# Optimization experiments

Measured on AMD Instinct MI355X. Metric: run time of the kernel, lower is better.

## Reference

```python
import jax, jax.numpy as jnp
import numpy as np

B, S, D = 2, 2048, 1024
H = 16
HD = D // H  # head_dim = 64
NEG = -1e30  # finite stand-in for -inf; masked entries are zeroed after softmax so math matches


def setup_inputs() -> dict:
    key = jax.random.key(0)
    ks = jax.random.split(key, 10)
    q = jax.random.normal(ks[0], (B, S, D), dtype=jnp.float32)
    k = jax.random.normal(ks[1], (B, S, D), dtype=jnp.float32)
    v = jax.random.normal(ks[2], (B, S, D), dtype=jnp.float32)
    mask = jax.random.randint(ks[3], (B, S), 0, 2).astype(bool)
    s = 1.0 / np.sqrt(D)
    Wq = jax.random.uniform(ks[4], (D, D), jnp.float32, -s, s)
    bq = jax.random.uniform(ks[5], (D,), jnp.float32, -s, s)
    Wk = jax.random.uniform(ks[6], (D, D), jnp.float32, -s, s)
    bk = jax.random.uniform(ks[7], (D,), jnp.float32, -s, s)
    Wv = jax.random.uniform(ks[8], (D, D), jnp.float32, -s, s)
    bv = jax.random.uniform(ks[9], (D,), jnp.float32, -s, s)
    return {"q": q, "k": k, "v": v, "mask": mask,
            "Wq": Wq, "bq": bq, "Wk": Wk, "bk": bk, "Wv": Wv, "bv": bv}


def _split_heads(x):
    # [B,S,D] -> [H,B,S,HD]  (matches permute(2,0,1,3) in torch)
    return x.reshape(B, S, H, HD).transpose(2, 0, 1, 3)


def reference(q, k, v, mask, Wq, bq, Wk, bk, Wv, bv):
    mq = _split_heads(q @ Wq.T + bq)
    mk = _split_heads(k @ Wk.T + bk)
    mv = _split_heads(v @ Wv.T + bv)
    # scores: [H,B,Sq,Sk]
    scores = jnp.einsum('hbqd,hbkd->hbqk', mq, mk) / jnp.sqrt(jnp.float32(HD))
    pair_mask = (mask[:, :, None] & mask[:, None, :])[None]  # [1,B,S,S]
    scores = jnp.where(pair_mask, scores, NEG)
    attn = jax.nn.softmax(scores, axis=-1)
    attn = jnp.where(pair_mask, attn, 0.0)
    out = jnp.einsum('hbqk,hbkd->hbqd', attn, mv)
    # [H,B,S,HD] -> [B,S,D]
    return out.transpose(1, 2, 0, 3).reshape(B, S, H * HD)
```

## Files before the change

### kernel.cpp

```cpp
#include <hip/hip_runtime.h>
#include <math.h>

#define B_ 2
#define S_ 2048
#define D_ 1024
#define H_ 16
#define HD_ 64
#define LOG2E 1.44269504088896340736f

typedef __bf16 bf16_t;
typedef bf16_t bf16x8 __attribute__((ext_vector_type(8)));
typedef bf16_t bf16x4v __attribute__((ext_vector_type(4)));
typedef float f32x4 __attribute__((ext_vector_type(4)));

#define GLOBAL_LOAD_LDS16(gp, lp)                                              \
    __builtin_amdgcn_global_load_lds(                                          \
        (const __attribute__((address_space(1))) void*)(gp),                   \
        (__attribute__((address_space(3))) void*)(lp), 16, 0, 0)

__global__ __launch_bounds__(256) void cvt_kernel(
    const float* __restrict__ q, const float* __restrict__ k,
    const float* __restrict__ v, const float* __restrict__ wq,
    const float* __restrict__ wk, const float* __restrict__ wv,
    const int* __restrict__ msk,
    bf16_t* __restrict__ qb, bf16_t* __restrict__ kb, bf16_t* __restrict__ vb,
    bf16_t* __restrict__ wqb, bf16_t* __restrict__ wkb, bf16_t* __restrict__ wvb,
    float* __restrict__ kbias)
{
    const int y = blockIdx.y;
    size_t idx = ((size_t)blockIdx.x * 256 + threadIdx.x) * 4;

    if (y == 6) {
        if (idx >= (size_t)B_ * S_) return;
        int4 mi = *(const int4*)(msk + idx);
        float4 o4;
        const float VB = -8.0f * LOG2E;
        const float MB = -1.44269504e30f;
        o4.x = mi.x ? VB : MB;
        o4.y = mi.y ? VB : MB;
        o4.z = mi.z ? VB : MB;
        o4.w = mi.w ? VB : MB;
        *(float4*)(kbias + idx) = o4;
        return;
    }

    const float* src;
    bf16_t* dst;
    size_t n;
    switch (y) {
        case 0: src = q;  dst = qb;  n = (size_t)B_ * S_ * D_; break;
        case 1: src = k;  dst = kb;  n = (size_t)B_ * S_ * D_; break;
        case 2: src = v;  dst = vb;  n = (size_t)B_ * S_ * D_; break;
        case 3: src = wq; dst = wqb; n = (size_t)D_ * D_;      break;
        case 4: src = wk; dst = wkb; n = (size_t)D_ * D_;      break;
        default: src = wv; dst = wvb; n = (size_t)D_ * D_;     break;
    }
    if (idx >= n) return;
    float4 f = *(const float4*)(src + idx);
    bf16x4v o;
    o[0] = (bf16_t)f.x; o[1] = (bf16_t)f.y;
    o[2] = (bf16_t)f.z; o[3] = (bf16_t)f.w;
    *(bf16x4v*)(dst + idx) = o;
}

__global__ __launch_bounds__(256) void proj_mfma(
    const bf16_t* __restrict__ X0, const bf16_t* __restrict__ X1,
    const bf16_t* __restrict__ X2, const bf16_t* __restrict__ W0,
    const bf16_t* __restrict__ W1, const bf16_t* __restrict__ W2,
    const float* __restrict__ b0, const float* __restrict__ b1,
    const float* __restrict__ b2, bf16_t* __restrict__ o0,
    bf16_t* __restrict__ o1, bf16_t* __restrict__ o2)
{
    __shared__ __align__(16) bf16_t As[2][128 * 32];
    __shared__ __align__(16) bf16_t Bs[2][128 * 32];

    const int orig = blockIdx.x + 32 * blockIdx.y + 256 * blockIdx.z;
    const int work = (orig & 7) * 96 + (orig >> 3);
    const int bx = work & 31;
    const int by = (work >> 5) & 7;
    const int z  = work >> 8;

    const bf16_t* X = (z == 0) ? X0 : (z == 1) ? X1 : X2;
    const bf16_t* W = (z == 0) ? W0 : (z == 1) ? W1 : W2;
    const float* bias = (z == 0) ? b0 : (z == 1) ? b1 : b2;
    bf16_t* out = (z == 0) ? o0 : (z == 1) ? o1 : o2;
    const float oscale = (z == 0) ? (0.125f * LOG2E) : 1.0f;

    const int tid  = threadIdx.x;
    const int w    = tid >> 6;
    const int lane = tid & 63;
    const int L    = lane & 15;
    const int quad = lane >> 4;
    const int wr   = (w >> 1) * 64;
    const int wc   = (w & 1) * 64;
    const int row0 = bx * 128;
    const int col0 = by * 128;

    const int lr = lane >> 2;
    const int lc = (lane & 3) * 8;

    f32x4 acc[4][4];
    #pragma unroll
    for (int i = 0; i < 4; ++i)
        #pragma unroll
        for (int j = 0; j < 4; ++j) {
            acc[i][j][0] = 0.f; acc[i][j][1] = 0.f;
            acc[i][j][2] = 0.f; acc[i][j][3] = 0.f;
        }

    for (int k0 = 0; k0 < D_; k0 += 64) {
        __syncthreads();
        #pragma unroll
        for (int i = 0; i < 2; ++i) {
            const int rA = i * 64 + w * 16;
            const size_t xoff = (size_t)(row0 + rA + lr) * D_ + k0 + lc;
            const size_t woff = (size_t)(col0 + rA + lr) * D_ + k0 + lc;
            GLOBAL_LOAD_LDS16(X + xoff,      &As[0][rA * 32]);
            GLOBAL_LOAD_LDS16(X + xoff + 32, &As[1][rA * 32]);
            GLOBAL_LOAD_LDS16(W + woff,      &Bs[0][rA * 32]);
            GLOBAL_LOAD_LDS16(W + woff + 32, &Bs[1][rA * 32]);
        }
        __syncthreads();

        #pragma unroll
        for (int hh = 0; hh < 2; ++hh) {
            bf16x8 aF[4], bF[4];
            #pragma unroll
            for (int t = 0; t < 4; ++t) {
                aF[t] = *(const bf16x8*)&As[hh][(wr + t * 16 + L) * 32 + quad * 8];
                bF[t] = *(const bf16x8*)&Bs[hh][(wc + t * 16 + L) * 32 + quad * 8];
            }
            #pragma unroll
            for (int mt = 0; mt < 4; ++mt)
                #pragma unroll
                for (int nt = 0; nt < 4; ++nt)
                    acc[mt][nt] = __builtin_amdgcn_mfma_f32_16x16x32_bf16(
                        aF[mt], bF[nt], acc[mt][nt], 0, 0, 0);
        }
    }

    #pragma unroll
    for (int nt = 0; nt < 4; ++nt) {
        const int j  = col0 + wc + nt * 16 + L;
        const float bval = bias[j];
        const int h  = j >> 6;
        const int hd = j & 63;
        #pragma unroll
        for (int mt = 0; mt < 4; ++mt)
            #pragma unroll
            for (int r = 0; r < 4; ++r) {
                const int n = row0 + wr + mt * 16 + quad * 4 + r;
                const int b = n >> 11;
                const int s = n & (S_ - 1);
                out[((((size_t)b * H_ + h) * S_ + s) * HD_) + hd] =
                    (bf16_t)((acc[mt][nt][r] + bval) * oscale);
            }
    }
}

__global__ __launch_bounds__(256) void transpose_v(
    const bf16_t* __restrict__ mv, bf16_t* __restrict__ vt)
{
    __shared__ bf16_t tile[64][72];
    const int s0 = blockIdx.x * 64;
    const int bh = blockIdx.y;
    const int t  = threadIdx.x;

    const bf16_t* src = mv + ((size_t)bh * S_ + s0) * HD_;
    {
        int srow = t >> 2, c16 = (t & 3) * 16;
        bf16x8 a = *(const bf16x8*)(src + srow * HD_ + c16);
        bf16x8 b = *(const bf16x8*)(src + srow * HD_ + c16 + 8);
        *(bf16x8*)&tile[srow][c16]     = a;
        *(bf16x8*)&tile[srow][c16 + 8] = b;
    }
    __syncthreads();

    const int d  = t & 63;
    const int sc = (t >> 6) * 16;
    unsigned int w[8];
    #pragma unroll
    for (int j = 0; j < 8; ++j) {
        unsigned short lo = *(const unsigned short*)&tile[sc + 2*j][d];
        unsigned short hi = *(const unsigned short*)&tile[sc + 2*j + 1][d];
        w[j] = (unsigned int)lo | ((unsigned int)hi << 16);
    }
    bf16_t* dst = vt + ((size_t)bh * HD_ + d) * S_ + s0 + sc;
    uint4 u0; u0.x = w[0]; u0.y = w[1]; u0.z = w[2]; u0.w = w[3];
    uint4 u1; u1.x = w[4]; u1.y = w[5]; u1.z = w[6]; u1.w = w[7];
    ((uint4*)dst)[0] = u0;
    ((uint4*)dst)[1] = u1;
}

__global__ __launch_bounds__(256) void attn_kernel(
    const bf16_t* __restrict__ Q, const bf16_t* __restrict__ K,
    const bf16_t* __restrict__ Vt, const float* __restrict__ kbias,
    const int* __restrict__ mask, float* __restrict__ out)
{
    constexpr int LD = 72;
    __shared__ bf16_t Ks[64 * LD];
    __shared__ bf16_t Vs[64 * LD];
    __shared__ bf16_t Pt[4][32 * LD];

    const int tid  = threadIdx.x;
    const int w    = tid >> 6;
    const int lane = tid & 63;
    const int L    = lane & 15;
    const int quad = lane >> 4;

    const int orig = blockIdx.x + 16 * blockIdx.y + 256 * blockIdx.z;
    const int work = (orig & 7) * 64 + (orig >> 3);
    const int h    = (work >> 4) & 15;
    const int b    = work >> 8;
    const int bh   = b * H_ + h;
    const int q0   = (work & 15) * 128;

    const bf16_t* kbase = K  + (size_t)bh * S_ * HD_;
    const bf16_t* vbase = Vt + (size_t)bh * HD_ * S_;
    const float*  bbase = kbias + b * S_;
    const int*    mrow  = mask + b * S_;

    const int sr = tid >> 3;
    const int sc2 = (tid & 7) * 8;

    bf16x8 aQ[2][2];
    #pragma unroll
    for (int qb = 0; qb < 2; ++qb) {
        const bf16_t* qp = Q + ((size_t)bh * S_ + q0 + w * 32 + qb * 16 + L) * HD_;
        aQ[qb][0] = *(const bf16x8*)(qp + quad * 8);
        aQ[qb][1] = *(const bf16x8*)(qp + 32 + quad * 8);
    }

    f32x4 o[2][4];
    #pragma unroll
    for (int qb = 0; qb < 2; ++qb)
        #pragma unroll
        for (int f = 0; f < 4; ++f) {
            o[qb][f][0]=0.f; o[qb][f][1]=0.f; o[qb][f][2]=0.f; o[qb][f][3]=0.f;
        }
    float l_[2] = {0.f, 0.f};

    bf16x8 kr0, kr1, vr0, vr1;
    f32x4  bias_n[4];
    {
        kr0 = *(const bf16x8*)(kbase + (size_t)sr * HD_ + sc2);
        kr1 = *(const bf16x8*)(kbase + (size_t)(sr + 32) * HD_ + sc2);
        vr0 = *(const bf16x8*)(vbase + (size_t)sr * S_ + sc2);
        vr1 = *(const bf16x8*)(vbase + (size_t)(sr + 32) * S_ + sc2);
        #pragma unroll
        for (int f = 0; f < 4; ++f)
            bias_n[f] = *(const f32x4*)(bbase + f * 16 + quad * 4);
    }

    for (int kt = 0; kt < S_; kt += 64) {
        __syncthreads();
        *(bf16x8*)&Ks[sr * LD + sc2]        = kr0;
        *(bf16x8*)&Ks[(sr + 32) * LD + sc2] = kr1;
        *(bf16x8*)&Vs[sr * LD + sc2]        = vr0;
        *(bf16x8*)&Vs[(sr + 32) * LD + sc2] = vr1;
        f32x4 bias_c[4];
        #pragma unroll
        for (int f = 0; f < 4; ++f) bias_c[f] = bias_n[f];
        __syncthreads();

        if (kt + 64 < S_) {
            const int kn = kt + 64;
            kr0 = *(const bf16x8*)(kbase + (size_t)(kn + sr) * HD_ + sc2);
            kr1 = *(const bf16x8*)(kbase + (size_t)(kn + sr + 32) * HD_ + sc2);
            vr0 = *(const bf16x8*)(vbase + (size_t)sr * S_ + kn + sc2);
            vr1 = *(const bf16x8*)(vbase + (size_t)(sr + 32) * S_ + kn + sc2);
            #pragma unroll
            for (int f = 0; f < 4; ++f)
                bias_n[f] = *(const f32x4*)(bbase + kn + f * 16 + quad * 4);
        }

        bf16x8 aK[4][2];
        #pragma unroll
        for (int f = 0; f < 4; ++f) {
            aK[f][0] = *(const bf16x8*)&Ks[(f * 16 + L) * LD + quad * 8];
            aK[f][1] = *(const bf16x8*)&Ks[(f * 16 + L) * LD + 32 + quad * 8];
        }

        bf16_t* pw = &Pt[w][0];
        #pragma unroll
        for (int qb = 0; qb < 2; ++qb) {
            #pragma unroll
            for (int f = 0; f < 4; ++f) {
                f32x4 z = bias_c[f];
                z = __builtin_amdgcn_mfma_f32_16x16x32_bf16(aK[f][0], aQ[qb][0], z, 0, 0, 0);
                z = __builtin_amdgcn_mfma_f32_16x16x32_bf16(aK[f][1], aQ[qb][1], z, 0, 0, 0);
                float e0 = exp2f(z[0]);
                float e1 = exp2f(z[1]);
                float e2 = exp2f(z[2]);
                float e3 = exp2f(z[3]);
                l_[qb] += (e0 + e1) + (e2 + e3);
                bf16x4v p4;
                p4[0] = (bf16_t)e0; p4[1] = (bf16_t)e1;
                p4[2] = (bf16_t)e2; p4[3] = (bf16_t)e3;
                *(bf16x4v*)&pw[(qb * 16 + L) * LD + f * 16 + quad * 4] = p4;
            }
        }

        bf16x8 aP[2][2];
        #pragma unroll
        for (int qb = 0; qb < 2; ++qb) {
            aP[qb][0] = *(const bf16x8*)&pw[(qb * 16 + L) * LD + quad * 8];
            aP[qb][1] = *(const bf16x8*)&pw[(qb * 16 + L) * LD + 32 + quad * 8];
        }

        #pragma unroll
        for (int f = 0; f < 4; ++f) {
            bf16x8 bV0 = *(const bf16x8*)&Vs[(f * 16 + L) * LD + quad * 8];
            bf16x8 bV1 = *(const bf16x8*)&Vs[(f * 16 + L) * LD + 32 + quad * 8];
            #pragma unroll
            for (int qb = 0; qb < 2; ++qb) {
                o[qb][f] = __builtin_amdgcn_mfma_f32_16x16x32_bf16(aP[qb][0], bV0, o[qb][f], 0, 0, 0);
                o[qb][f] = __builtin_amdgcn_mfma_f32_16x16x32_bf16(aP[qb][1], bV1, o[qb][f], 0, 0, 0);
            }
        }
    }

    #pragma unroll
    for (int qb = 0; qb < 2; ++qb) {
        float t = l_[qb];
        t += __shfl_xor(t, 16);
        t += __shfl_xor(t, 32);
        int qv = mrow[q0 + w * 32 + qb * 16 + L];
        l_[qb] = (qv && t > 0.f) ? (1.0f / t) : 0.0f;
    }

    #pragma unroll
    for (int qb = 0; qb < 2; ++qb) {
        float inv[4];
        #pragma unroll
        for (int r = 0; r < 4; ++r)
            inv[r] = __shfl(l_[qb], quad * 4 + r);
        float* obase = out + ((size_t)b * S_ + q0 + w * 32 + qb * 16 + quad * 4) * D_ + h * HD_;
        #pragma unroll
        for (int f = 0; f < 4; ++f)
            #pragma unroll
            for (int r = 0; r < 4; ++r)
                obase[r * D_ + f * 16 + L] = o[qb][f][r] * inv[r];
    }
}

extern "C" void kernel_launch(void* const* d_in, const int* in_sizes, int n_in,
                              void* d_out, int out_size, void* d_ws, size_t ws_size,
                              hipStream_t stream)
{
    const float* q    = (const float*)d_in[0];
    const float* k    = (const float*)d_in[1];
    const float* v    = (const float*)d_in[2];
    const int*   mask = (const int*)d_in[3];
    const float* Wq   = (const float*)d_in[4];
    const float* bq   = (const float*)d_in[5];
    const float* Wk   = (const float*)d_in[6];
    const float* bk   = (const float*)d_in[7];
    const float* Wv   = (const float*)d_in[8];
    const float* bv   = (const float*)d_in[9];
    float* out = (float*)d_out;

    const size_t PE = (size_t)B_ * S_ * D_;
    const size_t WE = (size_t)D_ * D_;

    bf16_t* qb    = (bf16_t*)d_ws;
    bf16_t* kb    = qb + PE;
    bf16_t* vb    = kb + PE;
    bf16_t* wqb   = vb + PE;
    bf16_t* wkb   = wqb + WE;
    bf16_t* wvb   = wkb + WE;
    bf16_t* mq    = wvb + WE;
    bf16_t* mk    = mq + PE;
    bf16_t* mv    = mk + PE;
    bf16_t* vt    = mv + PE;
    float*  kbias = (float*)(vt + PE);

    dim3 cgrid(PE / (256 * 4), 7);
    cvt_kernel<<<cgrid, 256, 0, stream>>>(q, k, v, Wq, Wk, Wv, mask,
                                          qb, kb, vb, wqb, wkb, wvb, kbias);

    dim3 pgrid(4096 / 128, 1024 / 128, 3);
    proj_mfma<<<pgrid, 256, 0, stream>>>(qb, kb, vb, wqb, wkb, wvb,
                                         bq, bk, bv, mq, mk, mv);

    dim3 tgrid(S_ / 64, B_ * H_);
    transpose_v<<<tgrid, 256, 0, stream>>>(mv, vt);

    dim3 agrid(S_ / 128, H_, B_);
    attn_kernel<<<agrid, 256, 0, stream>>>(mq, mk, vt, kbias, mask, out);
}
```

Baseline: 227.2 us.

## Fuse V transpose into projection epilogue, flatten cvt grid, add MFMA priority hints

The V projection now writes its output directly in transposed [b,h,hd,s] layout from the GEMM epilogue, which removes the separate transpose kernel and its extra round trip through global memory. The conversion kernel uses a compact 1D grid so no blocks exit idle. The projection K-step drops from 64 to 32 with a single LDS buffer, and the block-index swizzles in the projection and attention kernels are removed. The attention loop gains s_setprio around its MFMA sections and an unroll-2 hint. The smaller K-step doubles the barrier count per output tile, and dropping the swizzles may hurt L2 locality.

```diff
diff --git a/kernel.cpp b/kernel.cpp
--- a/kernel.cpp
+++ b/kernel.cpp
@@ -27,11 +27,28 @@
     bf16_t* __restrict__ wqb, bf16_t* __restrict__ wkb, bf16_t* __restrict__ wvb,
     float* __restrict__ kbias)
 {
-    const int y = blockIdx.y;
-    size_t idx = ((size_t)blockIdx.x * 256 + threadIdx.x) * 4;
-
-    if (y == 6) {
-        if (idx >= (size_t)B_ * S_) return;
+    const size_t NT = (size_t)1 << 20;
+    const size_t NW = (size_t)1 << 18;
+    size_t g = (size_t)blockIdx.x * 256 + threadIdx.x;
+
+    const float* src;
+    bf16_t* dst;
+    size_t off;
+    if (g < 3 * NT) {
+        int t = (int)(g >> 20);
+        off = (g & (NT - 1)) * 4;
+        src = (t == 0) ? q : (t == 1) ? k : v;
+        dst = (t == 0) ? qb : (t == 1) ? kb : vb;
+    } else if (g < 3 * NT + 3 * NW) {
+        size_t gw = g - 3 * NT;
+        int t = (int)(gw >> 18);
+        off = (gw & (NW - 1)) * 4;
+        src = (t == 0) ? wq : (t == 1) ? wk : wv;
+        dst = (t == 0) ? wqb : (t == 1) ? wkb : wvb;
+    } else {
+        size_t gm = g - (3 * NT + 3 * NW);
+        if (gm >= (size_t)B_ * S_ / 4) return;
+        size_t idx = gm * 4;
         int4 mi = *(const int4*)(msk + idx);
         float4 o4;
         const float VB = -8.0f * LOG2E;
@@ -44,23 +61,11 @@
         return;
     }
 
-    const float* src;
-    bf16_t* dst;
-    size_t n;
-    switch (y) {
-        case 0: src = q;  dst = qb;  n = (size_t)B_ * S_ * D_; break;
-        case 1: src = k;  dst = kb;  n = (size_t)B_ * S_ * D_; break;
-        case 2: src = v;  dst = vb;  n = (size_t)B_ * S_ * D_; break;
-        case 3: src = wq; dst = wqb; n = (size_t)D_ * D_;      break;
-        case 4: src = wk; dst = wkb; n = (size_t)D_ * D_;      break;
-        default: src = wv; dst = wvb; n = (size_t)D_ * D_;     break;
-    }
-    if (idx >= n) return;
-    float4 f = *(const float4*)(src + idx);
+    float4 f = *(const float4*)(src + off);
     bf16x4v o;
     o[0] = (bf16_t)f.x; o[1] = (bf16_t)f.y;
     o[2] = (bf16_t)f.z; o[3] = (bf16_t)f.w;
-    *(bf16x4v*)(dst + idx) = o;
+    *(bf16x4v*)(dst + off) = o;
 }
 
 __global__ __launch_bounds__(256) void proj_mfma(
@@ -71,15 +76,10 @@
     const float* __restrict__ b2, bf16_t* __restrict__ o0,
     bf16_t* __restrict__ o1, bf16_t* __restrict__ o2)
 {
-    __shared__ __align__(16) bf16_t As[2][128 * 32];
-    __shared__ __align__(16) bf16_t Bs[2][128 * 32];
-
-    const int orig = blockIdx.x + 32 * blockIdx.y + 256 * blockIdx.z;
-    const int work = (orig & 7) * 96 + (orig >> 3);
-    const int bx = work & 31;
-    const int by = (work >> 5) & 7;
-    const int z  = work >> 8;
-
+    __shared__ __align__(16) bf16_t As[128 * 32];
+    __shared__ __align__(16) bf16_t Bs[128 * 32];
+
+    const int z = blockIdx.z;
     const bf16_t* X = (z == 0) ? X0 : (z == 1) ? X1 : X2;
     const bf16_t* W = (z == 0) ? W0 : (z == 1) ? W1 : W2;
     const float* bias = (z == 0) ? b0 : (z == 1) ? b1 : b2;
@@ -93,8 +93,8 @@
     const int quad = lane >> 4;
     const int wr   = (w >> 1) * 64;
     const int wc   = (w & 1) * 64;
-    const int row0 = bx * 128;
-    const int col0 = by * 128;
+    const int row0 = blockIdx.x * 128;
+    const int col0 = blockIdx.y * 128;
 
     const int lr = lane >> 2;
     const int lc = (lane & 3) * 8;
@@ -108,88 +108,70 @@
             acc[i][j][2] = 0.f; acc[i][j][3] = 0.f;
         }
 
-    for (int k0 = 0; k0 < D_; k0 += 64) {
+    for (int k0 = 0; k0 < D_; k0 += 32) {
         __syncthreads();
         #pragma unroll
         for (int i = 0; i < 2; ++i) {
             const int rA = i * 64 + w * 16;
-            const size_t xoff = (size_t)(row0 + rA + lr) * D_ + k0 + lc;
-            const size_t woff = (size_t)(col0 + rA + lr) * D_ + k0 + lc;
-            GLOBAL_LOAD_LDS16(X + xoff,      &As[0][rA * 32]);
-            GLOBAL_LOAD_LDS16(X + xoff + 32, &As[1][rA * 32]);
-            GLOBAL_LOAD_LDS16(W + woff,      &Bs[0][rA * 32]);
-            GLOBAL_LOAD_LDS16(W + woff + 32, &Bs[1][rA * 32]);
+            GLOBAL_LOAD_LDS16(X + (size_t)(row0 + rA + lr) * D_ + k0 + lc,
+                              &As[rA * 32]);
+            GLOBAL_LOAD_LDS16(W + (size_t)(col0 + rA + lr) * D_ + k0 + lc,
+                              &Bs[rA * 32]);
         }
         __syncthreads();
 
-        #pragma unroll
-        for (int hh = 0; hh < 2; ++hh) {
-            bf16x8 aF[4], bF[4];
-            #pragma unroll
-            for (int t = 0; t < 4; ++t) {
-                aF[t] = *(const bf16x8*)&As[hh][(wr + t * 16 + L) * 32 + quad * 8];
-                bF[t] = *(const bf16x8*)&Bs[hh][(wc + t * 16 + L) * 32 + quad * 8];
+        bf16x8 aF[4], bF[4];
+        #pragma unroll
+        for (int t = 0; t < 4; ++t) {
+            aF[t] = *(const bf16x8*)&As[(wr + t * 16 + L) * 32 + quad * 8];
+            bF[t] = *(const bf16x8*)&Bs[(wc + t * 16 + L) * 32 + quad * 8];
+        }
+        #pragma unroll
+        for (int mt = 0; mt < 4; ++mt)
+            #pragma unroll
+            for (int nt = 0; nt < 4; ++nt)
+                acc[mt][nt] = __builtin_amdgcn_mfma_f32_16x16x32_bf16(
+                    aF[mt], bF[nt], acc[mt][nt], 0, 0, 0);
+    }
+
+    if (z == 2) {
+        #pragma unroll
+        for (int nt = 0; nt < 4; ++nt) {
+            const int j  = col0 + wc + nt * 16 + L;
+            const float bval = bias[j];
+            const int h  = j >> 6;
+            const int hd = j & 63;
+            #pragma unroll
+            for (int mt = 0; mt < 4; ++mt) {
+                const int n0 = row0 + wr + mt * 16 + quad * 4;
+                const int b  = n0 >> 11;
+                const int s  = n0 & (S_ - 1);
+                bf16x4v p;
+                #pragma unroll
+                for (int r = 0; r < 4; ++r)
+                    p[r] = (bf16_t)(acc[mt][nt][r] + bval);
+                *(bf16x4v*)(out + ((size_t)(b * H_ + h) * HD_ + hd) * S_ + s) = p;
             }
+        }
+    } else {
+        #pragma unroll
+        for (int nt = 0; nt < 4; ++nt) {
+            const int j  = col0 + wc + nt * 16 + L;
+            const float bval = bias[j];
+            const int h  = j >> 6;
+            const int hd = j & 63;
             #pragma unroll
             for (int mt = 0; mt < 4; ++mt)
                 #pragma unroll
-                for (int nt = 0; nt < 4; ++nt)
-                    acc[mt][nt] = __builtin_amdgcn_mfma_f32_16x16x32_bf16(
-                        aF[mt], bF[nt], acc[mt][nt], 0, 0, 0);
-        }
-    }
-
-    #pragma unroll
-    for (int nt = 0; nt < 4; ++nt) {
-        const int j  = col0 + wc + nt * 16 + L;
-        const float bval = bias[j];
-        const int h  = j >> 6;
-        const int hd = j & 63;
-        #pragma unroll
-        for (int mt = 0; mt < 4; ++mt)
-            #pragma unroll
-            for (int r = 0; r < 4; ++r) {
-                const int n = row0 + wr + mt * 16 + quad * 4 + r;
-                const int b = n >> 11;
-                const int s = n & (S_ - 1);
-                out[((((size_t)b * H_ + h) * S_ + s) * HD_) + hd] =
-                    (bf16_t)((acc[mt][nt][r] + bval) * oscale);
-            }
-    }
-}
-
-__global__ __launch_bounds__(256) void transpose_v(
-    const bf16_t* __restrict__ mv, bf16_t* __restrict__ vt)
-{
-    __shared__ bf16_t tile[64][72];
-    const int s0 = blockIdx.x * 64;
-    const int bh = blockIdx.y;
-    const int t  = threadIdx.x;
-
-    const bf16_t* src = mv + ((size_t)bh * S_ + s0) * HD_;
-    {
-        int srow = t >> 2, c16 = (t & 3) * 16;
-        bf16x8 a = *(const bf16x8*)(src + srow * HD_ + c16);
-        bf16x8 b = *(const bf16x8*)(src + srow * HD_ + c16 + 8);
-        *(bf16x8*)&tile[srow][c16]     = a;
-        *(bf16x8*)&tile[srow][c16 + 8] = b;
-    }
-    __syncthreads();
-
-    const int d  = t & 63;
-    const int sc = (t >> 6) * 16;
-    unsigned int w[8];
-    #pragma unroll
-    for (int j = 0; j < 8; ++j) {
-        unsigned short lo = *(const unsigned short*)&tile[sc + 2*j][d];
-        unsigned short hi = *(const unsigned short*)&tile[sc + 2*j + 1][d];
-        w[j] = (unsigned int)lo | ((unsigned int)hi << 16);
-    }
-    bf16_t* dst = vt + ((size_t)bh * HD_ + d) * S_ + s0 + sc;
-    uint4 u0; u0.x = w[0]; u0.y = w[1]; u0.z = w[2]; u0.w = w[3];
-    uint4 u1; u1.x = w[4]; u1.y = w[5]; u1.z = w[6]; u1.w = w[7];
-    ((uint4*)dst)[0] = u0;
-    ((uint4*)dst)[1] = u1;
+                for (int r = 0; r < 4; ++r) {
+                    const int n = row0 + wr + mt * 16 + quad * 4 + r;
+                    const int b = n >> 11;
+                    const int s = n & (S_ - 1);
+                    out[((((size_t)b * H_ + h) * S_ + s) * HD_) + hd] =
+                        (bf16_t)((acc[mt][nt][r] + bval) * oscale);
+                }
+        }
+    }
 }
 
 __global__ __launch_bounds__(256) void attn_kernel(
@@ -207,13 +189,10 @@
     const int lane = tid & 63;
     const int L    = lane & 15;
     const int quad = lane >> 4;
-
-    const int orig = blockIdx.x + 16 * blockIdx.y + 256 * blockIdx.z;
-    const int work = (orig & 7) * 64 + (orig >> 3);
-    const int h    = (work >> 4) & 15;
-    const int b    = work >> 8;
+    const int h    = blockIdx.y;
+    const int b    = blockIdx.z;
     const int bh   = b * H_ + h;
-    const int q0   = (work & 15) * 128;
+    const int q0   = blockIdx.x * 128;
 
     const bf16_t* kbase = K  + (size_t)bh * S_ * HD_;
     const bf16_t* vbase = Vt + (size_t)bh * HD_ * S_;
@@ -252,6 +231,7 @@
             bias_n[f] = *(const f32x4*)(bbase + f * 16 + quad * 4);
     }
 
+    #pragma unroll 2
     for (int kt = 0; kt < S_; kt += 64) {
         __syncthreads();
         *(bf16x8*)&Ks[sr * LD + sc2]        = kr0;
@@ -287,8 +267,10 @@
             #pragma unroll
             for (int f = 0; f < 4; ++f) {
                 f32x4 z = bias_c[f];
+                __builtin_amdgcn_s_setprio(1);
                 z = __builtin_amdgcn_mfma_f32_16x16x32_bf16(aK[f][0], aQ[qb][0], z, 0, 0, 0);
                 z = __builtin_amdgcn_mfma_f32_16x16x32_bf16(aK[f][1], aQ[qb][1], z, 0, 0, 0);
+                __builtin_amdgcn_s_setprio(0);
                 float e0 = exp2f(z[0]);
                 float e1 = exp2f(z[1]);
                 float e2 = exp2f(z[2]);
@@ -308,6 +290,7 @@
             aP[qb][1] = *(const bf16x8*)&pw[(qb * 16 + L) * LD + 32 + quad * 8];
         }
 
+        __builtin_amdgcn_s_setprio(1);
         #pragma unroll
         for (int f = 0; f < 4; ++f) {
             bf16x8 bV0 = *(const bf16x8*)&Vs[(f * 16 + L) * LD + quad * 8];
@@ -318,6 +301,7 @@
                 o[qb][f] = __builtin_amdgcn_mfma_f32_16x16x32_bf16(aP[qb][1], bV1, o[qb][f], 0, 0, 0);
             }
         }
+        __builtin_amdgcn_s_setprio(0);
     }
 
     #pragma unroll
@@ -371,20 +355,17 @@
     bf16_t* wvb   = wkb + WE;
     bf16_t* mq    = wvb + WE;
     bf16_t* mk    = mq + PE;
-    bf16_t* mv    = mk + PE;
-    bf16_t* vt    = mv + PE;
+    bf16_t* vt    = mk + PE;
     float*  kbias = (float*)(vt + PE);
 
-    dim3 cgrid(PE / (256 * 4), 7);
+    const size_t ngroups = 3 * (PE / 4) + 3 * (WE / 4) + (size_t)B_ * S_ / 4;
+    dim3 cgrid((ngroups + 255) / 256);
     cvt_kernel<<<cgrid, 256, 0, stream>>>(q, k, v, Wq, Wk, Wv, mask,
                                           qb, kb, vb, wqb, wkb, wvb, kbias);
 
     dim3 pgrid(4096 / 128, 1024 / 128, 3);
     proj_mfma<<<pgrid, 256, 0, stream>>>(qb, kb, vb, wqb, wkb, wvb,
-                                         bq, bk, bv, mq, mk, mv);
-
-    dim3 tgrid(S_ / 64, B_ * H_);
-    transpose_v<<<tgrid, 256, 0, stream>>>(mv, vt);
+                                         bq, bk, bv, mq, mk, vt);
 
     dim3 agrid(S_ / 128, H_, B_);
     attn_kernel<<<agrid, 256, 0, stream>>>(mq, mk, vt, kbias, mask, out);
```

New measurement: 226.4 us. About the same (-0.4%).
